# Optimization experiments

Hardware: AMD Instinct MI355X
Metric: run time of the kernel (lower is better)

Reference implementation:

```python
import jax, jax.numpy as jnp
import numpy as np

HIDDEN = 1536
BOTTLENECK = 128
LN_EPS = 1e-5


def setup_inputs() -> dict:
    key = jax.random.key(0)
    k1, k2, k3 = jax.random.split(key, 3)
    hidden_states = jax.random.normal(k1, (4, 4096, HIDDEN), dtype=jnp.float32)
    # xavier_uniform with gain=0.01: bound = gain * sqrt(6/(fan_in+fan_out))
    bound = 0.01 * np.sqrt(6.0 / (HIDDEN + BOTTLENECK))
    w_down = jax.random.uniform(k2, (BOTTLENECK, HIDDEN), minval=-bound, maxval=bound, dtype=jnp.float32)
    w_up = jax.random.uniform(k3, (HIDDEN, BOTTLENECK), minval=-bound, maxval=bound, dtype=jnp.float32)
    ln_gamma = jnp.ones((HIDDEN,), dtype=jnp.float32)
    ln_beta = jnp.zeros((HIDDEN,), dtype=jnp.float32)
    return {"hidden_states": hidden_states, "w_down": w_down, "w_up": w_up,
            "ln_gamma": ln_gamma, "ln_beta": ln_beta}


def _fourier_2d(x):
    # fp32 FFT round-trip along seq (axis=1) then feature (axis=2), ortho norm
    orig_dtype = x.dtype
    xf = x.astype(jnp.float32)
    f = jnp.fft.fft(xf, axis=1, norm='ortho')
    f = jnp.fft.fft(f, axis=2, norm='ortho')
    t = jnp.fft.ifft(f, axis=2, norm='ortho')
    t = jnp.fft.ifft(t, axis=1, norm='ortho')
    return jnp.real(t).astype(orig_dtype)


def reference(hidden_states, w_down, w_up, ln_gamma, ln_beta):
    residual = hidden_states
    # down_proj: [b,s,H] @ [H,B] -> [b,s,B]   (nn.Linear uses x @ W^T)
    x = jnp.einsum('bsh,dh->bsd', hidden_states, w_down)
    # dropout is identity in eval mode
    x = _fourier_2d(x)
    # up_proj: [b,s,B] -> [b,s,H]
    x = jnp.einsum('bsd,hd->bsh', x, w_up)
    y = residual + x
    mu = jnp.mean(y, axis=-1, keepdims=True)
    var = jnp.mean(jnp.square(y - mu), axis=-1, keepdims=True)
    return (y - mu) * jax.lax.rsqrt(var + LN_EPS) * ln_gamma + ln_beta
```

## Files before the change

### kernel.cpp

```cpp
#include <hip/hip_runtime.h>

#define H 1536
#define BD 128
#define ROWS 16
#define NTHREADS 512
#define NBLOCKS 1024

using f16x8 = _Float16 __attribute__((ext_vector_type(8)));
using f32x4 = float __attribute__((ext_vector_type(4)));
using i64x2 = long __attribute__((ext_vector_type(2)));

#define WD_SCALE 16384.0f
#define T8_SCALE (1.0f/128.0f)
#define X_SCALE  (1.0f/2097152.0f)

__global__ __launch_bounds__(256) void pack_weights(const float* __restrict__ wd,
                                                    const float* __restrict__ wu,
                                                    char* __restrict__ wdp8,
                                                    char* __restrict__ wup8) {
    int f = blockIdx.x * 256 + threadIdx.x;
    const float* src;
    char* dst;
    if (f < 24576) {
        int w = f / 3072, rem = f - w * 3072;
        int ph = rem >> 6, l = rem & 63;
        int row = 16 * w + (l & 15);
        int col = 32 * ph + 8 * (l >> 4);
        src = wd + (size_t)row * H + col;
        int p = ph >> 1, half = ph & 1;
        dst = wdp8 + (((size_t)(w * 24 + p) * 64 + l) * 16 + half * 8);
    } else {
        int g = f - 24576;
        int w = g / 3072, rem = g - w * 3072;
        int t2 = rem >> 6, l = rem & 63;
        int nf = t2 >> 2, kf = t2 & 3;
        int row = 192 * w + 16 * nf + (l & 15);
        int col = 32 * kf + 8 * (l >> 4);
        src = wu + (size_t)row * BD + col;
        int q = nf * 2 + (kf >> 1), half = kf & 1;
        dst = wup8 + (((size_t)(w * 24 + q) * 64 + l) * 16 + half * 8);
    }
    float4 v0 = reinterpret_cast<const float4*>(src)[0];
    float4 v1 = reinterpret_cast<const float4*>(src)[1];
    int i0 = __builtin_amdgcn_cvt_pk_fp8_f32(v0.x * WD_SCALE, v0.y * WD_SCALE, 0, false);
    i0     = __builtin_amdgcn_cvt_pk_fp8_f32(v0.z * WD_SCALE, v0.w * WD_SCALE, i0, true);
    int i1 = __builtin_amdgcn_cvt_pk_fp8_f32(v1.x * WD_SCALE, v1.y * WD_SCALE, 0, false);
    i1     = __builtin_amdgcn_cvt_pk_fp8_f32(v1.z * WD_SCALE, v1.w * WD_SCALE, i1, true);
    int2 st = {i0, i1};
    *reinterpret_cast<int2*>(dst) = st;
}

__global__ __launch_bounds__(NTHREADS, 4) void fused_adapter(
    const float* __restrict__ hs,
    const char* __restrict__ wdp8,
    const char* __restrict__ wup8,
    const float* __restrict__ gamma,
    const float* __restrict__ beta,
    float* __restrict__ out)
{
    __shared__ alignas(16) char smem[75776];
    _Float16* hsb = reinterpret_cast<_Float16*>(smem);
    char* hsa8    = smem + 49152;
    char* tb8     = smem + 73728;
    float* redS   = reinterpret_cast<float*>(smem + 73728);
    float* redQ   = redS + 8 * ROWS;
    float* statsM = redQ + 8 * ROWS;
    float* statsR = statsM + ROWS;

    const int tid  = threadIdx.x;
    const int lane = tid & 63;
    const int w    = tid >> 6;
    const int l15  = lane & 15;
    const int lk   = lane >> 4;
    const long row0 = (long)blockIdx.x * ROWS;
    const float* hsblk = hs + row0 * H;

    const i64x2* wp2 = reinterpret_cast<const i64x2*>(wdp8) + (size_t)w * 24 * 64 + lane;
    const i64x2* up2 = reinterpret_cast<const i64x2*>(wup8) + (size_t)w * 24 * 64 + lane;

    i64x2 bq[4];
    bq[0] = wp2[0 * 64]; bq[1] = wp2[1 * 64]; bq[2] = wp2[2 * 64]; bq[3] = wp2[3 * 64];

    float4 va[6], vb[6];
    int rr[6], c8a[6];
#pragma unroll
    for (int i = 0; i < 6; ++i) {
        int c  = tid + NTHREADS * i;
        int r  = c / 192;
        int c8 = c - r * 192;
        rr[i] = r; c8a[i] = c8;
        const float4* p = reinterpret_cast<const float4*>(hsblk + (long)r * H + c8 * 8);
        va[i] = p[0];
        vb[i] = p[1];
    }
#pragma unroll
    for (int i = 0; i < 6; ++i) {
        int r = rr[i], c8 = c8a[i], col = c8 * 8;
        f16x8 hv;
        hv[0] = (_Float16)va[i].x; hv[1] = (_Float16)va[i].y;
        hv[2] = (_Float16)va[i].z; hv[3] = (_Float16)va[i].w;
        hv[4] = (_Float16)vb[i].x; hv[5] = (_Float16)vb[i].y;
        hv[6] = (_Float16)vb[i].z; hv[7] = (_Float16)vb[i].w;
        *reinterpret_cast<f16x8*>(&hsb[r * H + (col ^ ((r & 7) << 3))]) = hv;
        int j0 = __builtin_amdgcn_cvt_pk_fp8_f32(va[i].x, va[i].y, 0, false);
        j0     = __builtin_amdgcn_cvt_pk_fp8_f32(va[i].z, va[i].w, j0, true);
        int j1 = __builtin_amdgcn_cvt_pk_fp8_f32(vb[i].x, vb[i].y, 0, false);
        j1     = __builtin_amdgcn_cvt_pk_fp8_f32(vb[i].z, vb[i].w, j1, true);
        int kk = c8 >> 2, m = c8 & 3;
        int al = (16 * m + r) ^ ((kk & 15) << 1);
        int2 stv = {j0, j1};
        *reinterpret_cast<int2*>(&hsa8[(kk * 64 + al) * 8]) = stv;
    }
    __syncthreads();

    f32x4 accv[4] = {{0,0,0,0},{0,0,0,0},{0,0,0,0},{0,0,0,0}};
#pragma unroll
    for (int p = 0; p < 24; ++p) {
        int kk0 = 2 * p, kk1 = 2 * p + 1;
        long alo = *reinterpret_cast<const long*>(&hsa8[(kk0 * 64 + (lane ^ ((kk0 & 15) << 1))) * 8]);
        long ahi = *reinterpret_cast<const long*>(&hsa8[(kk1 * 64 + (lane ^ ((kk1 & 15) << 1))) * 8]);
        i64x2 b = bq[p & 3];
        if (p + 4 < 24) bq[p & 3] = wp2[(p + 4) * 64];
        f32x4 a = accv[p & 3];
        a = __builtin_amdgcn_mfma_f32_16x16x32_fp8_fp8(alo, b[0], a, 0, 0, 0);
        a = __builtin_amdgcn_mfma_f32_16x16x32_fp8_fp8(ahi, b[1], a, 0, 0, 0);
        accv[p & 3] = a;
    }

    i64x2 uq[4];
    uq[0] = up2[0 * 64]; uq[1] = up2[1 * 64]; uq[2] = up2[2 * 64]; uq[3] = up2[3 * 64];

    {
        f32x4 a1 = (accv[0] + accv[1]) + (accv[2] + accv[3]);
        int p0 = __builtin_amdgcn_cvt_pk_fp8_f32(a1[0] * T8_SCALE, a1[1] * T8_SCALE, 0, false);
        int p1 = __builtin_amdgcn_cvt_pk_fp8_f32(a1[2] * T8_SCALE, a1[3] * T8_SCALE, 0, false);
        int kk2 = w >> 1;
        int lane_hi = 2 * (w & 1) + (l15 >> 3);
        int e8 = l15 & 7;
        int base = (kk2 * 64 + 16 * lane_hi + 4 * lk) * 8 + e8;
        tb8[base + 0 * 8] = (char)(p0 & 0xFF);
        tb8[base + 1 * 8] = (char)((p0 >> 8) & 0xFF);
        tb8[base + 2 * 8] = (char)(p1 & 0xFF);
        tb8[base + 3 * 8] = (char)((p1 >> 8) & 0xFF);
    }
    __syncthreads();

    long a2f8[4];
#pragma unroll
    for (int kf = 0; kf < 4; ++kf)
        a2f8[kf] = *reinterpret_cast<const long*>(&tb8[(kf * 64 + lane) * 8]);
    __syncthreads();

    float sums[4] = {0.f, 0.f, 0.f, 0.f};
    float sumq[4] = {0.f, 0.f, 0.f, 0.f};
#pragma unroll
    for (int nf = 0; nf < 12; ++nf) {
        i64x2 u0 = uq[(2 * nf) & 3];
        i64x2 u1 = uq[(2 * nf + 1) & 3];
        if (2 * nf + 4 < 24) uq[(2 * nf) & 3]     = up2[(2 * nf + 4) * 64];
        if (2 * nf + 5 < 24) uq[(2 * nf + 1) & 3] = up2[(2 * nf + 5) * 64];
        f32x4 acc = {0.f, 0.f, 0.f, 0.f};
        acc = __builtin_amdgcn_mfma_f32_16x16x32_fp8_fp8(a2f8[0], u0[0], acc, 0, 0, 0);
        acc = __builtin_amdgcn_mfma_f32_16x16x32_fp8_fp8(a2f8[1], u0[1], acc, 0, 0, 0);
        acc = __builtin_amdgcn_mfma_f32_16x16x32_fp8_fp8(a2f8[2], u1[0], acc, 0, 0, 0);
        acc = __builtin_amdgcn_mfma_f32_16x16x32_fp8_fp8(a2f8[3], u1[1], acc, 0, 0, 0);
        int cn = 192 * w + 16 * nf + l15;
#pragma unroll
        for (int j = 0; j < 4; ++j) {
            int r = 4 * lk + j;
            int idx = r * H + (cn ^ ((r & 7) << 3));
            float y = acc[j] * X_SCALE + (float)hsb[idx];
            sums[j] += y;
            sumq[j] += y * y;
            hsb[idx] = (_Float16)y;
        }
    }

#pragma unroll
    for (int j = 0; j < 4; ++j) {
#pragma unroll
        for (int off = 1; off < 16; off <<= 1) {
            sums[j] += __shfl_xor(sums[j], off);
            sumq[j] += __shfl_xor(sumq[j], off);
        }
    }
    if (l15 == 0) {
#pragma unroll
        for (int j = 0; j < 4; ++j) {
            int r = 4 * lk + j;
            redS[w * ROWS + r] = sums[j];
            redQ[w * ROWS + r] = sumq[j];
        }
    }
    __syncthreads();
    if (tid < ROWS) {
        float S = 0.f, Q = 0.f;
#pragma unroll
        for (int ww = 0; ww < 8; ++ww) {
            S += redS[ww * ROWS + tid];
            Q += redQ[ww * ROWS + tid];
        }
        float mean = S * (1.0f / (float)H);
        float var  = Q * (1.0f / (float)H) - mean * mean;
        statsM[tid] = mean;
        statsR[tid] = rsqrtf(var + 1e-5f);
    }
    __syncthreads();

#pragma unroll
    for (int i = 0; i < 6; ++i) {
        int c  = tid + NTHREADS * i;
        int r  = c / 192;
        int c8 = c - r * 192;
        int col = c8 * 8;
        f16x8 yv = *reinterpret_cast<const f16x8*>(&hsb[r * H + (col ^ ((r & 7) << 3))]);
        float mean = statsM[r];
        float rstd = statsR[r];
        const float4* gp = reinterpret_cast<const float4*>(gamma + col);
        const float4* bp = reinterpret_cast<const float4*>(beta + col);
        float4 g0 = gp[0], g1 = gp[1];
        float4 b0 = bp[0], b1 = bp[1];
        float4 o0, o1;
        o0.x = ((float)yv[0] - mean) * rstd * g0.x + b0.x;
        o0.y = ((float)yv[1] - mean) * rstd * g0.y + b0.y;
        o0.z = ((float)yv[2] - mean) * rstd * g0.z + b0.z;
        o0.w = ((float)yv[3] - mean) * rstd * g0.w + b0.w;
        o1.x = ((float)yv[4] - mean) * rstd * g1.x + b1.x;
        o1.y = ((float)yv[5] - mean) * rstd * g1.y + b1.y;
        o1.z = ((float)yv[6] - mean) * rstd * g1.z + b1.z;
        o1.w = ((float)yv[7] - mean) * rstd * g1.w + b1.w;
        float4* op = reinterpret_cast<float4*>(out + (row0 + r) * H + col);
        op[0] = o0;
        op[1] = o1;
    }
}

extern "C" void kernel_launch(void* const* d_in, const int* in_sizes, int n_in,
                              void* d_out, int out_size, void* d_ws, size_t ws_size,
                              hipStream_t stream) {
    const float* hs    = (const float*)d_in[0];
    const float* wd    = (const float*)d_in[1];
    const float* wu    = (const float*)d_in[2];
    const float* gam   = (const float*)d_in[3];
    const float* bet   = (const float*)d_in[4];
    float* out = (float*)d_out;

    char* wdp8 = (char*)d_ws;
    char* wup8 = (char*)d_ws + (size_t)128 * H;

    pack_weights<<<192, 256, 0, stream>>>(wd, wu, wdp8, wup8);
    fused_adapter<<<NBLOCKS, NTHREADS, 0, stream>>>(hs, wdp8, wup8, gam, bet, out);
}
```

Baseline: 60.54 us.

## Keep input rows in registers and drop fp16 shared-memory copy of hidden states

The fp16 copy of the 16-row input tile in shared memory is removed. The fp32 input values stay in registers through the whole kernel, and the up-projection result is written to shared memory as scaled fp8. Each thread then adds it back to its own registers and computes LayerNorm statistics with full-wave shuffles. This shrinks shared memory from about 74KB to 26KB per block, which allows more resident blocks and removes the fp16 read-modify-write traffic. The cost is higher register pressure and fp8 quantisation of the adapter branch, which is tiny because of its scale.

```diff
diff --git a/kernel.cpp b/kernel.cpp
--- a/kernel.cpp
+++ b/kernel.cpp
@@ -12,7 +12,8 @@
 
 #define WD_SCALE 16384.0f
 #define T8_SCALE (1.0f/128.0f)
-#define X_SCALE  (1.0f/2097152.0f)
+#define X8_STORE (1.0f/16.0f)
+#define XF_SCALE (1.0f/131072.0f)
 
 __global__ __launch_bounds__(256) void pack_weights(const float* __restrict__ wd,
                                                     const float* __restrict__ wu,
@@ -58,14 +59,14 @@
     const float* __restrict__ beta,
     float* __restrict__ out)
 {
-    __shared__ alignas(16) char smem[75776];
-    _Float16* hsb = reinterpret_cast<_Float16*>(smem);
-    char* hsa8    = smem + 49152;
-    char* tb8     = smem + 73728;
-    float* redS   = reinterpret_cast<float*>(smem + 73728);
-    float* redQ   = redS + 8 * ROWS;
-    float* statsM = redQ + 8 * ROWS;
-    float* statsR = statsM + ROWS;
+    __shared__ alignas(16) char smem[26624];
+    char* hsa8    = smem;
+    char* x8      = smem;
+    char* tb8     = smem + 24576;
+    float* redS   = reinterpret_cast<float*>(smem + 24576);
+    float* redQ   = redS + 48;
+    float* statsM = redQ + 48;
+    float* statsR = statsM + 16;
 
     const int tid  = threadIdx.x;
     const int lane = tid & 63;
@@ -82,26 +83,20 @@
     bq[0] = wp2[0 * 64]; bq[1] = wp2[1 * 64]; bq[2] = wp2[2 * 64]; bq[3] = wp2[3 * 64];
 
     float4 va[6], vb[6];
-    int rr[6], c8a[6];
-#pragma unroll
-    for (int i = 0; i < 6; ++i) {
-        int c  = tid + NTHREADS * i;
-        int r  = c / 192;
-        int c8 = c - r * 192;
-        rr[i] = r; c8a[i] = c8;
+#pragma unroll
+    for (int i = 0; i < 6; ++i) {
+        int c  = tid + NTHREADS * i;
+        int r  = c / 192;
+        int c8 = c - r * 192;
         const float4* p = reinterpret_cast<const float4*>(hsblk + (long)r * H + c8 * 8);
         va[i] = p[0];
         vb[i] = p[1];
     }
 #pragma unroll
     for (int i = 0; i < 6; ++i) {
-        int r = rr[i], c8 = c8a[i], col = c8 * 8;
-        f16x8 hv;
-        hv[0] = (_Float16)va[i].x; hv[1] = (_Float16)va[i].y;
-        hv[2] = (_Float16)va[i].z; hv[3] = (_Float16)va[i].w;
-        hv[4] = (_Float16)vb[i].x; hv[5] = (_Float16)vb[i].y;
-        hv[6] = (_Float16)vb[i].z; hv[7] = (_Float16)vb[i].w;
-        *reinterpret_cast<f16x8*>(&hsb[r * H + (col ^ ((r & 7) << 3))]) = hv;
+        int c  = tid + NTHREADS * i;
+        int r  = c / 192;
+        int c8 = c - r * 192;
         int j0 = __builtin_amdgcn_cvt_pk_fp8_f32(va[i].x, va[i].y, 0, false);
         j0     = __builtin_amdgcn_cvt_pk_fp8_f32(va[i].z, va[i].w, j0, true);
         int j1 = __builtin_amdgcn_cvt_pk_fp8_f32(vb[i].x, vb[i].y, 0, false);
@@ -149,10 +144,7 @@
 #pragma unroll
     for (int kf = 0; kf < 4; ++kf)
         a2f8[kf] = *reinterpret_cast<const long*>(&tb8[(kf * 64 + lane) * 8]);
-    __syncthreads();
-
-    float sums[4] = {0.f, 0.f, 0.f, 0.f};
-    float sumq[4] = {0.f, 0.f, 0.f, 0.f};
+
 #pragma unroll
     for (int nf = 0; nf < 12; ++nf) {
         i64x2 u0 = uq[(2 * nf) & 3];
@@ -165,41 +157,54 @@
         acc = __builtin_amdgcn_mfma_f32_16x16x32_fp8_fp8(a2f8[2], u1[0], acc, 0, 0, 0);
         acc = __builtin_amdgcn_mfma_f32_16x16x32_fp8_fp8(a2f8[3], u1[1], acc, 0, 0, 0);
         int cn = 192 * w + 16 * nf + l15;
-#pragma unroll
-        for (int j = 0; j < 4; ++j) {
-            int r = 4 * lk + j;
-            int idx = r * H + (cn ^ ((r & 7) << 3));
-            float y = acc[j] * X_SCALE + (float)hsb[idx];
-            sums[j] += y;
-            sumq[j] += y * y;
-            hsb[idx] = (_Float16)y;
+        int p0 = __builtin_amdgcn_cvt_pk_fp8_f32(acc[0] * X8_STORE, acc[1] * X8_STORE, 0, false);
+        int p1 = __builtin_amdgcn_cvt_pk_fp8_f32(acc[2] * X8_STORE, acc[3] * X8_STORE, 0, false);
+        x8[(4 * lk + 0) * H + cn] = (char)(p0 & 0xFF);
+        x8[(4 * lk + 1) * H + cn] = (char)((p0 >> 8) & 0xFF);
+        x8[(4 * lk + 2) * H + cn] = (char)(p1 & 0xFF);
+        x8[(4 * lk + 3) * H + cn] = (char)(p1 >> 8 & 0xFF);
+    }
+    __syncthreads();
+
+    float sums[6], sumq[6];
+#pragma unroll
+    for (int i = 0; i < 6; ++i) {
+        int c  = tid + NTHREADS * i;
+        int r  = c / 192;
+        int c8 = c - r * 192;
+        int2 xw = *reinterpret_cast<const int2*>(&x8[r * H + c8 * 8]);
+        va[i].x += __builtin_amdgcn_cvt_f32_fp8(xw.x, 0) * XF_SCALE;
+        va[i].y += __builtin_amdgcn_cvt_f32_fp8(xw.x, 1) * XF_SCALE;
+        va[i].z += __builtin_amdgcn_cvt_f32_fp8(xw.x, 2) * XF_SCALE;
+        va[i].w += __builtin_amdgcn_cvt_f32_fp8(xw.x, 3) * XF_SCALE;
+        vb[i].x += __builtin_amdgcn_cvt_f32_fp8(xw.y, 0) * XF_SCALE;
+        vb[i].y += __builtin_amdgcn_cvt_f32_fp8(xw.y, 1) * XF_SCALE;
+        vb[i].z += __builtin_amdgcn_cvt_f32_fp8(xw.y, 2) * XF_SCALE;
+        vb[i].w += __builtin_amdgcn_cvt_f32_fp8(xw.y, 3) * XF_SCALE;
+        float s = (va[i].x + va[i].y) + (va[i].z + va[i].w)
+                + (vb[i].x + vb[i].y) + (vb[i].z + vb[i].w);
+        float q = (va[i].x * va[i].x + va[i].y * va[i].y)
+                + (va[i].z * va[i].z + va[i].w * va[i].w)
+                + (vb[i].x * vb[i].x + vb[i].y * vb[i].y)
+                + (vb[i].z * vb[i].z + vb[i].w * vb[i].w);
+        sums[i] = s; sumq[i] = q;
+    }
+#pragma unroll
+    for (int i = 0; i < 6; ++i) {
+#pragma unroll
+        for (int off = 1; off < 64; off <<= 1) {
+            sums[i] += __shfl_xor(sums[i], off);
+            sumq[i] += __shfl_xor(sumq[i], off);
         }
-    }
-
-#pragma unroll
-    for (int j = 0; j < 4; ++j) {
-#pragma unroll
-        for (int off = 1; off < 16; off <<= 1) {
-            sums[j] += __shfl_xor(sums[j], off);
-            sumq[j] += __shfl_xor(sumq[j], off);
+        if (lane == 0) {
+            redS[w + 8 * i] = sums[i];
+            redQ[w + 8 * i] = sumq[i];
         }
     }
-    if (l15 == 0) {
-#pragma unroll
-        for (int j = 0; j < 4; ++j) {
-            int r = 4 * lk + j;
-            redS[w * ROWS + r] = sums[j];
-            redQ[w * ROWS + r] = sumq[j];
-        }
-    }
     __syncthreads();
     if (tid < ROWS) {
-        float S = 0.f, Q = 0.f;
-#pragma unroll
-        for (int ww = 0; ww < 8; ++ww) {
-            S += redS[ww * ROWS + tid];
-            Q += redQ[ww * ROWS + tid];
-        }
+        float S = redS[3 * tid] + redS[3 * tid + 1] + redS[3 * tid + 2];
+        float Q = redQ[3 * tid] + redQ[3 * tid + 1] + redQ[3 * tid + 2];
         float mean = S * (1.0f / (float)H);
         float var  = Q * (1.0f / (float)H) - mean * mean;
         statsM[tid] = mean;
@@ -213,7 +218,6 @@
         int r  = c / 192;
         int c8 = c - r * 192;
         int col = c8 * 8;
-        f16x8 yv = *reinterpret_cast<const f16x8*>(&hsb[r * H + (col ^ ((r & 7) << 3))]);
         float mean = statsM[r];
         float rstd = statsR[r];
         const float4* gp = reinterpret_cast<const float4*>(gamma + col);
@@ -221,14 +225,14 @@
         float4 g0 = gp[0], g1 = gp[1];
         float4 b0 = bp[0], b1 = bp[1];
         float4 o0, o1;
-        o0.x = ((float)yv[0] - mean) * rstd * g0.x + b0.x;
-        o0.y = ((float)yv[1] - mean) * rstd * g0.y + b0.y;
-        o0.z = ((float)yv[2] - mean) * rstd * g0.z + b0.z;
-        o0.w = ((float)yv[3] - mean) * rstd * g0.w + b0.w;
-        o1.x = ((float)yv[4] - mean) * rstd * g1.x + b1.x;
-        o1.y = ((float)yv[5] - mean) * rstd * g1.y + b1.y;
-        o1.z = ((float)yv[6] - mean) * rstd * g1.z + b1.z;
-        o1.w = ((float)yv[7] - mean) * rstd * g1.w + b1.w;
+        o0.x = (va[i].x - mean) * rstd * g0.x + b0.x;
+        o0.y = (va[i].y - mean) * rstd * g0.y + b0.y;
+        o0.z = (va[i].z - mean) * rstd * g0.z + b0.z;
+        o0.w = (va[i].w - mean) * rstd * g0.w + b0.w;
+        o1.x = (vb[i].x - mean) * rstd * g1.x + b1.x;
+        o1.y = (vb[i].y - mean) * rstd * g1.y + b1.y;
+        o1.z = (vb[i].z - mean) * rstd * g1.z + b1.z;
+        o1.w = (vb[i].w - mean) * rstd * g1.w + b1.w;
         float4* op = reinterpret_cast<float4*>(out + (row0 + r) * H + col);
         op[0] = o0;
         op[1] = o1;
```

Measured after the change: 80.12 us. 1.32x slower.
